# Performance work log

Hardware: AMD Instinct MI355X
Metric: run time of the kernel (lower is better)

Reference implementation:

```python
import jax, jax.numpy as jnp
import numpy as np

T, N, C = 1024, 4, 4
RADIUS, COMPRESSION = 256, 1
TAU = 2.0  # LIF filter time constant (LIF_Filter source unavailable; exponential leaky integrator assumed)


def _build_delay():
    # Mirrors JeffressFilter.__init__ delay construction exactly.
    neg = np.arange(-RADIUS, 0, COMPRESSION, dtype=np.int64)
    pos = np.arange(RADIUS, 0, -COMPRESSION, dtype=np.int64)[::-1]
    _d = np.concatenate([neg, pos]).reshape(-1, 1)            # (D_out, 1)
    delay = np.maximum(np.concatenate([_d, -_d], axis=1), 0)  # relu -> (D_out, 2)
    return jnp.asarray(delay, dtype=jnp.int32)


def setup_inputs() -> dict:
    key = jax.random.key(0)
    k1, k2 = jax.random.split(key)
    x = jax.random.normal(k1, (T, N, C, 2), dtype=jnp.float32)
    delay = _build_delay()                                   # (D_out, 2) int
    d_out = delay.shape[0]                                   # 512
    # get_weight(1.0, 10.0, compression) source unavailable; stand-in float vector per output channel
    weight = jax.random.normal(k2, (d_out,), dtype=jnp.float32)
    return {"x": x, "weight": weight, "delay": delay}


def _lif_filter(x):
    # Leaky integrator over time axis 0: v[t] = exp(-1/tau) * v[t-1] + x[t]
    decay = jnp.asarray(np.exp(-1.0 / TAU), dtype=x.dtype)

    def step(v, xt):
        v = decay * v + xt
        return v, v

    _, y = jax.lax.scan(step, jnp.zeros(x.shape[1:], x.dtype), x)
    return y  # (T, N, C, 2)


def reference(x, weight, delay):
    Tlen = x.shape[0]
    y = _lif_filter(x)                                       # (T, N, C, 2)

    t = jnp.arange(Tlen, dtype=jnp.int32)
    # SpikeDelay.forward: mask rows t >= T - delay to 0, then gather at (t - delay) % T.
    # Equivalent post-gather: out[t] = y[t - delay] if t >= delay else 0 (zero-padded shift).
    t_idx = (t[:, None, None] - delay[None]) % Tlen          # (T, D_out, 2)
    i_idx = jnp.arange(2, dtype=jnp.int32)[None, None, :]    # broadcast over (T, D_out, 2)
    yt = jnp.moveaxis(y, -1, 1)                              # (T, 2, N, C)
    gathered = yt[t_idx, i_idx]                              # (T, D_out, 2, N, C)
    mask = t[:, None, None] >= delay[None]                   # (T, D_out, 2)
    out = jnp.where(mask[..., None, None], gathered, 0.0)
    out = out.sum(axis=2)                                    # sum over in_features=2 -> (T, D_out, N, C)
    out = jnp.moveaxis(out, 1, -1)                           # (T, N, C, D_out)
    return out * weight                                      # scale per output channel
```

## Files before the change

kernel.cpp:

```cpp
#include <hip/hip_runtime.h>


#define T_LEN  1024
#define D_OUT  512
#define T_TILE 16
#define WIN    (256 + T_TILE)

__global__ __launch_bounds__(512) void lif_scan_kernel(const float* __restrict__ x,
                                                       float* __restrict__ y) {
    const int tid   = threadIdx.x;
    const int ch    = tid & 31;
    const int chunk = tid >> 5;
    const int t0    = chunk * 64;
    const float decay = 0.60653065971263342f;

    float v = 0.0f;
    #pragma unroll 8
    for (int k = 0; k < 64; ++k) {
        int t = t0 - 64 + k;
        float xv = (t >= 0) ? x[t * 32 + ch] : 0.0f;
        v = decay * v + xv;
    }
    #pragma unroll 8
    for (int k = 0; k < 64; ++k) {
        int t = t0 + k;
        v = decay * v + x[t * 32 + ch];
        y[t * 32 + ch] = v;
    }
}

__global__ __launch_bounds__(256) void jeffress_kernel(const float* __restrict__ y,
                                                       const float* __restrict__ w,
                                                       const int* __restrict__ delay,
                                                       float4* __restrict__ out) {
    __shared__ float y0[WIN];
    __shared__ float y1[WIN];

    const int bid = blockIdx.x;
    const int nc  = bid & 15;
    const int t0  = (bid >> 4) * T_TILE;
    const int tid = threadIdx.x;

    for (int k = tid; k < WIN; k += 256) {
        const int tg = t0 - 256 + k;
        float a = 0.0f, b = 0.0f;
        if (tg >= 0) {
            const float2 v = *(const float2*)(y + tg * 32 + nc * 2);
            a = v.x; b = v.y;
        }
        y0[k] = a;
        y1[k] = b;
    }
    __syncthreads();

    const int d4 = tid & 127;
    const int d  = d4 * 4;
    const int th = tid >> 7;

    const int4* dp = (const int4*)(delay + 2 * d);
    const int4 del01 = dp[0];
    const int4 del23 = dp[1];
    const float4 wv = ((const float4*)w)[d4];

    float4* outb = out + nc * (D_OUT / 4) + d4;

    #pragma unroll
    for (int j = 0; j < T_TILE / 2; ++j) {
        const int tl = th * (T_TILE / 2) + j;
        const int tr = 256 + tl;
        float4 o;
        o.x = wv.x * (y0[tr - del01.x] + y1[tr - del01.y]);
        o.y = wv.y * (y0[tr - del01.z] + y1[tr - del01.w]);
        o.z = wv.z * (y0[tr - del23.x] + y1[tr - del23.y]);
        o.w = wv.w * (y0[tr - del23.z] + y1[tr - del23.w]);
        outb[(t0 + tl) * 16 * (D_OUT / 4)] = o;
    }
}

extern "C" void kernel_launch(void* const* d_in, const int* in_sizes, int n_in,
                              void* d_out, int out_size, void* d_ws, size_t ws_size,
                              hipStream_t stream) {
    const float* x      = (const float*)d_in[0];
    const float* weight = (const float*)d_in[1];
    const int*   delay  = (const int*)d_in[2];
    float* out = (float*)d_out;
    float* y   = (float*)d_ws;

    lif_scan_kernel<<<1, 512, 0, stream>>>(x, y);

    const int nblocks = (T_LEN / T_TILE) * 16;
    jeffress_kernel<<<nblocks, 256, 0, stream>>>(y, weight, delay, (float4*)out);
}
```

Measured before the change: 81.39 us.

## Transpose LIF output to zero-padded per-channel rows and drop shared-memory staging

The scan kernel now writes y into a transposed workspace with one contiguous time row per (nc, input) channel, preceded by 256 zero-padding entries that the scan blocks clear. The scan is also spread across 16 blocks instead of one. The Jeffress kernel then reads the delayed values straight from global memory (L1/L2) through per-delay pointers. This removes the LDS fill, the __syncthreads, and the bounds checks. In exchange the reads are uncoalesced, data-dependent gathers from global memory instead of shared-memory reads.

```diff
diff --git a/kernel.cpp b/kernel.cpp
--- a/kernel.cpp
+++ b/kernel.cpp
@@ -3,77 +3,81 @@
 
 #define T_LEN  1024
 #define D_OUT  512
-#define T_TILE 16
-#define WIN    (256 + T_TILE)
+#define NC     16
+#define PAD    256
+#define ROW    (PAD + T_LEN)
+#define YB_OFF (NC * ROW)
 
-__global__ __launch_bounds__(512) void lif_scan_kernel(const float* __restrict__ x,
-                                                       float* __restrict__ y) {
-    const int tid   = threadIdx.x;
-    const int ch    = tid & 31;
-    const int chunk = tid >> 5;
-    const int t0    = chunk * 64;
-    const float decay = 0.60653065971263342f;
+__global__ __launch_bounds__(64) void lif_scan_kernel(const float* __restrict__ x,
+                                                      float* __restrict__ ws) {
+    const int tid = threadIdx.x;
+    const int b   = blockIdx.x;
 
-    float v = 0.0f;
-    #pragma unroll 8
-    for (int k = 0; k < 64; ++k) {
-        int t = t0 - 64 + k;
-        float xv = (t >= 0) ? x[t * 32 + ch] : 0.0f;
-        v = decay * v + xv;
+    #pragma unroll
+    for (int k = 0; k < 8; ++k) {
+        const int id = (b * 64 + tid) * 8 + k;
+        const int r  = id >> 8;
+        const int c  = id & 255;
+        ws[r * ROW + c] = 0.0f;
     }
-    #pragma unroll 8
-    for (int k = 0; k < 64; ++k) {
-        int t = t0 + k;
-        v = decay * v + x[t * 32 + ch];
-        y[t * 32 + ch] = v;
+
+    if (tid < 32) {
+        const int ch = tid;
+        const int nc = ch >> 1;
+        const int i  = ch & 1;
+        float* row = ws + (i ? YB_OFF : 0) + nc * ROW + PAD;
+
+        const int   t0    = b * 64;
+        const float decay = 0.60653065971263342f;
+
+        float v = 0.0f;
+        #pragma unroll 8
+        for (int k = 0; k < 64; ++k) {
+            const int t = t0 - 64 + k;
+            const float xv = (t >= 0) ? x[t * 32 + ch] : 0.0f;
+            v = decay * v + xv;
+        }
+        #pragma unroll 8
+        for (int k = 0; k < 64; ++k) {
+            const int t = t0 + k;
+            v = decay * v + x[t * 32 + ch];
+            row[t] = v;
+        }
     }
 }
 
-__global__ __launch_bounds__(256) void jeffress_kernel(const float* __restrict__ y,
+__global__ __launch_bounds__(256) void jeffress_kernel(const float* __restrict__ ws,
                                                        const float* __restrict__ w,
                                                        const int* __restrict__ delay,
                                                        float4* __restrict__ out) {
-    __shared__ float y0[WIN];
-    __shared__ float y1[WIN];
-
     const int bid = blockIdx.x;
     const int nc  = bid & 15;
-    const int t0  = (bid >> 4) * T_TILE;
-    const int tid = threadIdx.x;
+    const int t0  = (bid >> 4) * 16 + (threadIdx.x >> 7) * 8;
+    const int d4  = threadIdx.x & 127;
+    const int d   = d4 * 4;
 
-    for (int k = tid; k < WIN; k += 256) {
-        const int tg = t0 - 256 + k;
-        float a = 0.0f, b = 0.0f;
-        if (tg >= 0) {
-            const float2 v = *(const float2*)(y + tg * 32 + nc * 2);
-            a = v.x; b = v.y;
-        }
-        y0[k] = a;
-        y1[k] = b;
-    }
-    __syncthreads();
+    const int4*   dp  = (const int4*)(delay + 2 * d);
+    const int4    e01 = dp[0];
+    const int4    e23 = dp[1];
+    const float4  wv  = ((const float4*)w)[d4];
 
-    const int d4 = tid & 127;
-    const int d  = d4 * 4;
-    const int th = tid >> 7;
+    const float* A = ws + nc * ROW + PAD + t0;
+    const float* B = ws + YB_OFF + nc * ROW + PAD + t0;
+    const float* a0 = A - e01.x;  const float* b0 = B - e01.y;
+    const float* a1 = A - e01.z;  const float* b1 = B - e01.w;
+    const float* a2 = A - e23.x;  const float* b2 = B - e23.y;
+    const float* a3 = A - e23.z;  const float* b3 = B - e23.w;
 
-    const int4* dp = (const int4*)(delay + 2 * d);
-    const int4 del01 = dp[0];
-    const int4 del23 = dp[1];
-    const float4 wv = ((const float4*)w)[d4];
-
-    float4* outb = out + nc * (D_OUT / 4) + d4;
+    float4* op = out + (size_t)t0 * (NC * D_OUT / 4) + nc * (D_OUT / 4) + d4;
 
     #pragma unroll
-    for (int j = 0; j < T_TILE / 2; ++j) {
-        const int tl = th * (T_TILE / 2) + j;
-        const int tr = 256 + tl;
+    for (int j = 0; j < 8; ++j) {
         float4 o;
-        o.x = wv.x * (y0[tr - del01.x] + y1[tr - del01.y]);
-        o.y = wv.y * (y0[tr - del01.z] + y1[tr - del01.w]);
-        o.z = wv.z * (y0[tr - del23.x] + y1[tr - del23.y]);
-        o.w = wv.w * (y0[tr - del23.z] + y1[tr - del23.w]);
-        outb[(t0 + tl) * 16 * (D_OUT / 4)] = o;
+        o.x = wv.x * (a0[j] + b0[j]);
+        o.y = wv.y * (a1[j] + b1[j]);
+        o.z = wv.z * (a2[j] + b2[j]);
+        o.w = wv.w * (a3[j] + b3[j]);
+        op[j * (NC * D_OUT / 4)] = o;
     }
 }
 
@@ -84,10 +88,10 @@
     const float* weight = (const float*)d_in[1];
     const int*   delay  = (const int*)d_in[2];
     float* out = (float*)d_out;
-    float* y   = (float*)d_ws;
+    float* ws  = (float*)d_ws;
 
-    lif_scan_kernel<<<1, 512, 0, stream>>>(x, y);
+    lif_scan_kernel<<<16, 64, 0, stream>>>(x, ws);
 
-    const int nblocks = (T_LEN / T_TILE) * 16;
-    jeffress_kernel<<<nblocks, 256, 0, stream>>>(y, weight, delay, (float4*)out);
+    const int nblocks = (T_LEN / 16) * NC;
+    jeffress_kernel<<<nblocks, 256, 0, stream>>>(ws, weight, delay, (float4*)out);
 }
```

After: 78.66 us. 1.03x faster.
